# Optimization experiments

Hardware: AMD Instinct MI355X
Metric: run time of the kernel (lower is better)

Reference implementation:

```python
import jax, jax.numpy as jnp
import numpy as np

DIM = 1024; DEPTH = 2; DSTATE = 128; HEADDIM = 64; DCONV = 4; EXPAND = 2
DINNER = EXPAND * DIM; NHEADS = DINNER // HEADDIM
CONVCH = DINNER + 2 * DSTATE          # x, B, C channels fed through depthwise conv
DINPROJ = 2 * DINNER + 2 * DSTATE + NHEADS  # z, xBC, dt
VOCAB = 256; EPS = 1e-5
B, T = 2, 1024


def _causal_conv(x, w, b):
    # depthwise causal conv1d: x [B,T,C], w [C,K], b [C]
    K = w.shape[1]
    xp = jnp.pad(x, ((0, 0), (K - 1, 0), (0, 0)))
    y = jnp.broadcast_to(b, x.shape)
    for k in range(K):
        y = y + xp[:, k:k + x.shape[1], :] * w[:, k]
    return y


def _mamba2_layer(h, Wp, cw, cb, dtb, alog, Dd, gw, Wo):
    Bb, Tt, _ = h.shape
    zxbcdt = jnp.einsum('btd,pd->btp', h, Wp)   # [B,T,DINPROJ]
    z = zxbcdt[..., :DINNER]
    xBC = zxbcdt[..., DINNER:DINNER + CONVCH]
    dt_raw = zxbcdt[..., DINNER + CONVCH:]
    xBC = jax.nn.silu(_causal_conv(xBC, cw, cb))
    xs = xBC[..., :DINNER].reshape(Bb, Tt, NHEADS, HEADDIM)
    Bm = xBC[..., DINNER:DINNER + DSTATE]        # [B,T,N] (ngroups=1)
    Cm = xBC[..., DINNER + DSTATE:]              # [B,T,N]
    dt = jax.nn.softplus(dt_raw + dtb)           # [B,T,H]
    dA = jnp.exp(dt * (-jnp.exp(alog)))          # [B,T,H]

    def step(s, inps):
        da_t, dt_t, x_t, b_t, c_t = inps
        dbx = dt_t[:, :, None, None] * x_t[..., None] * b_t[:, None, None, :]
        s = da_t[:, :, None, None] * s + dbx     # [B,H,P,N]
        y = jnp.einsum('bhpn,bn->bhp', s, c_t)
        return s, y

    s0 = jnp.zeros((Bb, NHEADS, HEADDIM, DSTATE), h.dtype)
    seq = (jnp.moveaxis(dA, 1, 0), jnp.moveaxis(dt, 1, 0), jnp.moveaxis(xs, 1, 0),
           jnp.moveaxis(Bm, 1, 0), jnp.moveaxis(Cm, 1, 0))
    _, ys = jax.lax.scan(step, s0, seq)          # ys [T,B,H,P]
    y = jnp.moveaxis(ys, 0, 1) + Dd[:, None] * xs
    y = y.reshape(Bb, Tt, DINNER) * jax.nn.silu(z)   # gated RMSNorm (norm(y*silu(z)))
    y = y * jax.lax.rsqrt(jnp.mean(y * y, -1, keepdims=True) + EPS) * gw
    return jnp.einsum('bti,di->btd', y, Wo)


def setup_inputs() -> dict:
    key = jax.random.key(0)
    ks = jax.random.split(key, 8)
    s = 0.02
    inp = {}
    inp['x'] = jax.random.randint(ks[0], (B, T), 0, VOCAB)
    inp['embed'] = jax.random.normal(ks[1], (VOCAB, DIM)) * s
    inp['in_proj_w'] = jax.random.normal(ks[2], (DEPTH, DINPROJ, DIM)) * s
    inp['conv_w'] = jax.random.normal(ks[3], (DEPTH, CONVCH, DCONV)) * 0.2
    inp['conv_b'] = jnp.zeros((DEPTH, CONVCH))
    # dt_bias so softplus(dt) ~ [1e-3, 1e-1]
    inp['dt_bias'] = jax.random.uniform(ks[4], (DEPTH, NHEADS), minval=-4.6, maxval=-2.0)
    inp['A_log'] = jnp.log(jnp.broadcast_to(jnp.arange(1, NHEADS + 1, dtype=jnp.float32), (DEPTH, NHEADS)))
    inp['D'] = jnp.ones((DEPTH, NHEADS))
    inp['gnorm_w'] = jnp.ones((DEPTH, DINNER))
    inp['out_proj_w'] = jax.random.normal(ks[5], (DEPTH, DIM, DINNER)) * s
    inp['final_norm_w'] = jnp.ones((DIM,))
    return inp


def reference(x, embed, in_proj_w, conv_w, conv_b, dt_bias, A_log, D, gnorm_w, out_proj_w, final_norm_w):
    h = embed[x]                                  # [B,T,DIM]
    for l in range(DEPTH):
        h = h + _mamba2_layer(h, in_proj_w[l], conv_w[l], conv_b[l], dt_bias[l],
                              A_log[l], D[l], gnorm_w[l], out_proj_w[l])
    h = h * jax.lax.rsqrt(jnp.mean(h * h, -1, keepdims=True) + EPS) * final_norm_w
    return jnp.einsum('btd,vd->btv', h, embed)    # tied head -> logits [B,T,256]
```

## Files before the change

### kernel.cpp

```cpp
#include <hip/hip_runtime.h>
#include <hip/hip_bf16.h>

#define BT 2048
#define T_SEQ 1024
#define DIM 1024
#define DINNER 2048
#define DSTATE 128
#define HEADDIM 64
#define NHEADS 32
#define CONVCH 2304
#define DINPROJ 4384
#define EPS_F 1e-5f
#define NCHUNK 16

typedef __bf16 bf16x8 __attribute__((ext_vector_type(8)));
typedef float f32x4 __attribute__((ext_vector_type(4)));

__device__ __forceinline__ float b2f(unsigned short u) {
  union { unsigned int i; float f; } v; v.i = ((unsigned int)u) << 16; return v.f;
}
__device__ __forceinline__ unsigned short f2b(float f) {
  unsigned int x = __float_as_uint(f);
  return (unsigned short)((x + 0x7fffu + ((x >> 16) & 1u)) >> 16);
}

__device__ __forceinline__ void gload_lds16(const void* g, void* l) {
  __builtin_amdgcn_global_load_lds(
      (const __attribute__((address_space(1))) unsigned int*)g,
      (__attribute__((address_space(3))) unsigned int*)l, 16, 0, 0);
}

#define NWP_ELEM (2 * DINPROJ * DIM)
#define NWO_ELEM (2 * DIM * DINNER)
#define NEM_ELEM (256 * DIM)
#define NWP_BLK (NWP_ELEM / 4 / 256)
#define NWO_BLK (NWO_ELEM / 4 / 256)
#define NEM_BLK (NEM_ELEM / 4 / 256)
#define PRO_BLK (NWP_BLK + NWO_BLK + NEM_BLK + BT)

__global__ void prologue_k(const float* __restrict__ Wp, const float* __restrict__ Wo,
                           const float* __restrict__ emb, const float* __restrict__ gw,
                           unsigned short* __restrict__ Wp_b,
                           unsigned short* __restrict__ Wo_b,
                           unsigned short* __restrict__ emb_b,
                           const int* __restrict__ x,
                           float* __restrict__ h, unsigned short* __restrict__ hb) {
  int bid = blockIdx.x;
  if (bid < NWP_BLK) {
    int i = (bid * 256 + threadIdx.x) * 4;
    float4 v = *(const float4*)(Wp + i);
    Wp_b[i + 0] = f2b(v.x); Wp_b[i + 1] = f2b(v.y);
    Wp_b[i + 2] = f2b(v.z); Wp_b[i + 3] = f2b(v.w);
  } else if (bid < NWP_BLK + NWO_BLK) {
    int i = ((bid - NWP_BLK) * 256 + threadIdx.x) * 4;
    int li = i / (DIM * DINNER);
    int kk = i & (DINNER - 1);
    float4 v = *(const float4*)(Wo + i);
    float4 g = *(const float4*)(gw + li * DINNER + kk);
    Wo_b[i + 0] = f2b(v.x * g.x); Wo_b[i + 1] = f2b(v.y * g.y);
    Wo_b[i + 2] = f2b(v.z * g.z); Wo_b[i + 3] = f2b(v.w * g.w);
  } else if (bid < NWP_BLK + NWO_BLK + NEM_BLK) {
    int i = ((bid - NWP_BLK - NWO_BLK) * 256 + threadIdx.x) * 4;
    float4 v = *(const float4*)(emb + i);
    emb_b[i + 0] = f2b(v.x); emb_b[i + 1] = f2b(v.y);
    emb_b[i + 2] = f2b(v.z); emb_b[i + 3] = f2b(v.w);
  } else {
    int t = bid - (NWP_BLK + NWO_BLK + NEM_BLK);
    int tok = x[t];
    int d = threadIdx.x;
#pragma unroll
    for (int j = 0; j < 4; ++j, d += 256) {
      float v = emb[(size_t)tok * DIM + d];
      h[(size_t)t * DIM + d] = v;
      hb[(size_t)t * DIM + d] = f2b(v);
    }
  }
}

template <int MODE, int TM, int TN>
__global__ __launch_bounds__(256) void gemm_bt(
    const unsigned short* __restrict__ A,
    const unsigned short* __restrict__ Bw,
    int M, int N, int K,
    unsigned short* __restrict__ Cout,
    float* __restrict__ aux,
    unsigned short* __restrict__ aux2,
    const float* __restrict__ ssq) {
  constexpr int FM = TM / 32, FN = TN / 32;
  constexpr int JA = TM / 64, JB = TN / 64;
  constexpr int HA = TM * 32, HB = TN * 32;
  __shared__ __align__(16) unsigned short As[2 * HA];
  __shared__ __align__(16) unsigned short Bs[2 * HB];
  const int tid = threadIdx.x;
  const int lane = tid & 63;
  const int wave = tid >> 6;

  const int gx = gridDim.x, gy = gridDim.y;
  const int nwg = gx * gy;
  const int orig = (int)(blockIdx.y * gx + blockIdx.x);
  const int q = nwg >> 3, rr = nwg & 7;
  const int xcd = orig & 7, idx = orig >> 3;
  const int swz = (xcd < rr ? xcd * (q + 1) : rr * (q + 1) + (xcd - rr) * q) + idx;
  const int bxs = swz / gy;
  const int bys = swz - bxs * gy;
  const int m0 = bys * TM;
  const int n0 = bxs * TN;

  const int wm = (wave >> 1) * (TM / 2);
  const int wn = (wave & 1) * (TN / 2);
  const int quad = lane >> 4;
  const int r = lane & 15;

  f32x4 acc[FM][FN];
#pragma unroll
  for (int i = 0; i < FM; ++i)
#pragma unroll
    for (int j = 0; j < FN; ++j) acc[i][j] = f32x4{0.f, 0.f, 0.f, 0.f};

  const int rowt = tid >> 2, colt = (tid & 3) * 8;
  const unsigned short* aG[JA];
  unsigned short* aD[JA];
  const unsigned short* bG[JB];
  unsigned short* bD[JB];
#pragma unroll
  for (int j = 0; j < JA; ++j) {
    aG[j] = A + (size_t)(m0 + rowt + j * 64) * K + colt;
    aD[j] = As + wave * 512 + j * 2048;
  }
#pragma unroll
  for (int j = 0; j < JB; ++j) {
    int rb = n0 + rowt + j * 64; if (rb >= N) rb = N - 1;
    bG[j] = Bw + (size_t)rb * K + colt;
    bD[j] = Bs + wave * 512 + j * 2048;
  }

#pragma unroll
  for (int j = 0; j < JA; ++j) gload_lds16(aG[j], aD[j]);
#pragma unroll
  for (int j = 0; j < JB; ++j) gload_lds16(bG[j], bD[j]);
  __syncthreads();

  int cur = 0;
  for (int k0 = 0; k0 < K; k0 += 32) {
    const int nxt = cur ^ 1;
    if (k0 + 32 < K) {
#pragma unroll
      for (int j = 0; j < JA; ++j) gload_lds16(aG[j] + k0 + 32, aD[j] + nxt * HA);
#pragma unroll
      for (int j = 0; j < JB; ++j) gload_lds16(bG[j] + k0 + 32, bD[j] + nxt * HB);
    }
    const bf16x8* ap = (const bf16x8*)(As + cur * HA);
    const bf16x8* bp = (const bf16x8*)(Bs + cur * HB);
    bf16x8 af[FM], bfr[FN];
#pragma unroll
    for (int mt = 0; mt < FM; ++mt) af[mt] = ap[(wm + mt * 16 + r) * 4 + quad];
#pragma unroll
    for (int nt = 0; nt < FN; ++nt) bfr[nt] = bp[(wn + nt * 16 + r) * 4 + quad];
#pragma unroll
    for (int mt = 0; mt < FM; ++mt)
#pragma unroll
      for (int nt = 0; nt < FN; ++nt)
        acc[mt][nt] = __builtin_amdgcn_mfma_f32_16x16x32_bf16(af[mt], bfr[nt], acc[mt][nt], 0, 0, 0);
    __syncthreads();
    cur = nxt;
  }

#pragma unroll
  for (int mt = 0; mt < FM; ++mt) {
#pragma unroll
    for (int nt = 0; nt < FN; ++nt) {
#pragma unroll
      for (int i = 0; i < 4; ++i) {
        int gm = m0 + wm + mt * 16 + quad * 4 + i;
        int gn = n0 + wn + nt * 16 + r;
        if (gn < N) {
          float v = acc[mt][nt][i];
          if (MODE == 0) {
            Cout[(size_t)gm * N + gn] = f2b(v);
            if (gn >= DINNER + CONVCH)
              aux[(size_t)gm * NHEADS + (gn - (DINNER + CONVCH))] = v;
          } else if (MODE == 1) {
            float scl = rsqrtf(ssq[gm] * (1.f / DINNER) + EPS_F);
            size_t o = (size_t)gm * N + gn;
            float hnv = aux[o] + v * scl;
            aux[o] = hnv;
            aux2[o] = f2b(hnv);
          } else {
            aux[(size_t)gm * N + gn] = v;
          }
        }
      }
    }
  }
}

__global__ void conv_k(const unsigned short* __restrict__ zx,
                       const float* __restrict__ cw,
                       const float* __restrict__ cb,
                       unsigned short* __restrict__ xbc,
                       unsigned short* __restrict__ bcb,
                       const float* __restrict__ dtraw,
                       const float* __restrict__ dtb,
                       const float* __restrict__ alog,
                       float* __restrict__ dtf,
                       float* __restrict__ lnAf,
                       float* __restrict__ ssq) {
  int t = blockIdx.x;
  int tt = t & (T_SEQ - 1);
  if (threadIdx.x == 0) ssq[t] = 0.f;
  if (threadIdx.x < NHEADS) {
    int h = threadIdx.x;
    float xx = dtraw[t * NHEADS + h] + dtb[h];
    float sp = (xx > 20.f) ? xx : log1pf(expf(xx));
    dtf[t * NHEADS + h] = sp;
    lnAf[t * NHEADS + h] = -sp * expf(alog[h]);
  }
  for (int c = threadIdx.x; c < CONVCH; c += 256) {
    float acc = cb[c];
#pragma unroll
    for (int k = 0; k < 4; ++k) {
      int tp = tt - 3 + k;
      if (tp >= 0)
        acc += b2f(zx[(size_t)(t - 3 + k) * DINPROJ + DINNER + c]) * cw[c * 4 + k];
    }
    float s = acc / (1.f + expf(-acc));
    unsigned short sb = f2b(s);
    xbc[(size_t)t * CONVCH + c] = sb;
    if (c >= DINNER) bcb[(size_t)t * 256 + (c - DINNER)] = sb;
  }
}

__global__ __launch_bounds__(256) void ssd_intra(
    const unsigned short* __restrict__ bcb,
    const unsigned short* __restrict__ xbc,
    const float* __restrict__ dtf, const float* __restrict__ lnAf,
    unsigned short* __restrict__ y1buf, unsigned short* __restrict__ SL,
    float* __restrict__ dtot) {
  const int bi = blockIdx.x;
  const int c = bi & 15;
  const int h = (bi >> 4) & 31;
  const int b = bi >> 9;
  const int tid = threadIdx.x;
  const int w = tid >> 6, l = tid & 63, r = l & 15, quad = l >> 4;
  const size_t tok0 = (size_t)b * T_SEQ + c * 64;

  __shared__ __align__(16) unsigned short BCs[64 * 264];
  __shared__ __align__(16) unsigned short Xrow[64 * 72];
  __shared__ __align__(16) unsigned short XTs[64 * 72];
  __shared__ __align__(16) unsigned short BWT[128 * 72];
  __shared__ __align__(16) unsigned short Ms[64 * 72];
  __shared__ float cumL[64], dtL[64], wsL[64];

#pragma unroll
  for (int i = 0; i < 8; ++i) {
    int idx = tid + i * 256;
    int row = idx >> 5, col = (idx & 31) * 8;
    uint4 v = *(const uint4*)(bcb + (tok0 + row) * 256 + col);
    *(uint4*)(BCs + row * 264 + col) = v;
  }
#pragma unroll
  for (int i = 0; i < 2; ++i) {
    int idx = tid + i * 256;
    int u = idx >> 3, pc = (idx & 7) * 8;
    uint4 v = *(const uint4*)(xbc + (tok0 + u) * CONVCH + h * HEADDIM + pc);
    *(uint4*)(Xrow + u * 72 + pc) = v;
  }
  if (tid < 64) {
    float dt = dtf[(tok0 + tid) * NHEADS + h];
    float v = lnAf[(tok0 + tid) * NHEADS + h];
    dtL[tid] = dt;
#pragma unroll
    for (int off = 1; off < 64; off <<= 1) {
      float u = __shfl_up(v, off, 64);
      if (tid >= off) v += u;
    }
    cumL[tid] = v;
    float tot = __shfl(v, 63, 64);
    wsL[tid] = dt * expf(tot - v);
    if (tid == 63) dtot[bi] = expf(tot);
  }
  __syncthreads();

#pragma unroll
  for (int i = 0; i < 2; ++i) {
    int idx = tid + i * 256;
    int p = idx >> 3, ug = (idx & 7) * 8;
    unsigned short tA[8];
#pragma unroll
    for (int j = 0; j < 8; ++j) tA[j] = Xrow[(ug + j) * 72 + p];
    *(uint4*)(XTs + p * 72 + ug) = *(uint4*)tA;
  }

  {
    const int n = tid >> 1;
    const int ug = (tid & 1) * 32;
    unsigned short eb[32];
#pragma unroll
    for (int j = 0; j < 32; ++j)
      eb[j] = f2b(b2f(BCs[(ug + j) * 264 + n]) * wsL[ug + j]);
#pragma unroll
    for (int qq = 0; qq < 4; ++qq)
      *(uint4*)(BWT + n * 72 + ug + qq * 8) = *(uint4*)(eb + qq * 8);
  }

  f32x4 g[4];
#pragma unroll
  for (int nt = 0; nt < 4; ++nt) g[nt] = f32x4{0.f, 0.f, 0.f, 0.f};
#pragma unroll
  for (int kk = 0; kk < 4; ++kk) {
    bf16x8 afr = *(const bf16x8*)(BCs + (w * 16 + r) * 264 + 128 + kk * 32 + quad * 8);
#pragma unroll
    for (int nt = 0; nt < 4; ++nt) {
      bf16x8 bfr = *(const bf16x8*)(BCs + (nt * 16 + r) * 264 + kk * 32 + quad * 8);
      g[nt] = __builtin_amdgcn_mfma_f32_16x16x32_bf16(afr, bfr, g[nt], 0, 0, 0);
    }
  }
#pragma unroll
  for (int nt = 0; nt < 4; ++nt) {
#pragma unroll
    for (int i = 0; i < 4; ++i) {
      int t_ = w * 16 + quad * 4 + i;
      int u_ = nt * 16 + r;
      float wv = (u_ <= t_) ? expf(cumL[t_] - cumL[u_]) * dtL[u_] : 0.f;
      Ms[t_ * 72 + u_] = f2b(g[nt][i] * wv);
    }
  }
  __syncthreads();

  f32x4 y1[4];
#pragma unroll
  for (int nt = 0; nt < 4; ++nt) y1[nt] = f32x4{0.f, 0.f, 0.f, 0.f};
#pragma unroll
  for (int kk = 0; kk < 2; ++kk) {
    bf16x8 afr = *(const bf16x8*)(Ms + (w * 16 + r) * 72 + kk * 32 + quad * 8);
#pragma unroll
    for (int nt = 0; nt < 4; ++nt) {
      bf16x8 bfr = *(const bf16x8*)(XTs + (nt * 16 + r) * 72 + kk * 32 + quad * 8);
      y1[nt] = __builtin_amdgcn_mfma_f32_16x16x32_bf16(afr, bfr, y1[nt], 0, 0, 0);
    }
  }
#pragma unroll
  for (int nt = 0; nt < 4; ++nt)
#pragma unroll
    for (int i = 0; i < 4; ++i) {
      int t_ = w * 16 + quad * 4 + i, p_ = nt * 16 + r;
      y1buf[((size_t)bi * 64 + t_) * 64 + p_] = f2b(y1[nt][i]);
    }

  f32x4 sl[8];
#pragma unroll
  for (int nt = 0; nt < 8; ++nt) sl[nt] = f32x4{0.f, 0.f, 0.f, 0.f};
#pragma unroll
  for (int kk = 0; kk < 2; ++kk) {
    bf16x8 afr = *(const bf16x8*)(XTs + (w * 16 + r) * 72 + kk * 32 + quad * 8);
#pragma unroll
    for (int nt = 0; nt < 8; ++nt) {
      bf16x8 bfr = *(const bf16x8*)(BWT + (nt * 16 + r) * 72 + kk * 32 + quad * 8);
      sl[nt] = __builtin_amdgcn_mfma_f32_16x16x32_bf16(afr, bfr, sl[nt], 0, 0, 0);
    }
  }
#pragma unroll
  for (int nt = 0; nt < 8; ++nt)
#pragma unroll
    for (int i = 0; i < 4; ++i) {
      int p_ = w * 16 + quad * 4 + i, n_ = nt * 16 + r;
      SL[((size_t)bi * 64 + p_) * 128 + n_] = f2b(sl[nt][i]);
    }
}

__global__ void ssd_state(unsigned short* __restrict__ SL,
                          const float* __restrict__ dtot) {
  int gidx = blockIdx.x * 256 + threadIdx.x;
  int n4 = (gidx & 31) * 4;
  int p = (gidx >> 5) & 63;
  int bh = gidx >> 11;
  float sx = 0.f, sy = 0.f, sz = 0.f, sw = 0.f;
  for (int c = 0; c < NCHUNK; ++c) {
    size_t off = ((size_t)(bh * 16 + c) * 64 + p) * 128 + n4;
    uint2 lv = *(uint2*)(SL + off);
    float d = dtot[bh * 16 + c];
    uint2 sv;
    sv.x = (unsigned)f2b(sx) | ((unsigned)f2b(sy) << 16);
    sv.y = (unsigned)f2b(sz) | ((unsigned)f2b(sw) << 16);
    *(uint2*)(SL + off) = sv;
    sx = d * sx + b2f(lv.x & 0xffff);
    sy = d * sy + b2f(lv.x >> 16);
    sz = d * sz + b2f(lv.y & 0xffff);
    sw = d * sw + b2f(lv.y >> 16);
  }
}

__global__ __launch_bounds__(256) void ssd_inter(
    const unsigned short* __restrict__ bcb,
    const unsigned short* __restrict__ SL,
    const unsigned short* __restrict__ y1buf,
    const unsigned short* __restrict__ xbc,
    const unsigned short* __restrict__ zx,
    const float* __restrict__ lnAf,
    const float* __restrict__ Dw,
    unsigned short* __restrict__ yg,
    float* __restrict__ ssq) {
  const int bi = blockIdx.x;
  const int c = bi & 15, h = (bi >> 4) & 31, b = bi >> 9;
  const int tid = threadIdx.x;
  const int w = tid >> 6, l = tid & 63, r = l & 15, quad = l >> 4;
  const size_t tok0 = (size_t)b * T_SEQ + c * 64;

  __shared__ __align__(16) unsigned short Cs[64 * 136];
  __shared__ __align__(16) unsigned short Sp[64 * 136];
  __shared__ __align__(16) float Yf[64 * 68];
  __shared__ float cumL[64];

#pragma unroll
  for (int i = 0; i < 4; ++i) {
    int idx = tid + i * 256;
    int row = idx >> 4, col = (idx & 15) * 8;
    uint4 v = *(const uint4*)(bcb + (tok0 + row) * 256 + 128 + col);
    *(uint4*)(Cs + row * 136 + col) = v;
    uint4 s = *(const uint4*)(SL + ((size_t)bi * 64 + row) * 128 + col);
    *(uint4*)(Sp + row * 136 + col) = s;
  }
  if (tid < 64) {
    float v = lnAf[(tok0 + tid) * NHEADS + h];
#pragma unroll
    for (int off = 1; off < 64; off <<= 1) {
      float u = __shfl_up(v, off, 64);
      if (tid >= off) v += u;
    }
    cumL[tid] = v;
  }
  __syncthreads();

  f32x4 yi[4];
#pragma unroll
  for (int nt = 0; nt < 4; ++nt) yi[nt] = f32x4{0.f, 0.f, 0.f, 0.f};
#pragma unroll
  for (int kk = 0; kk < 4; ++kk) {
    bf16x8 afr = *(const bf16x8*)(Cs + (w * 16 + r) * 136 + kk * 32 + quad * 8);
#pragma unroll
    for (int nt = 0; nt < 4; ++nt) {
      bf16x8 bfr = *(const bf16x8*)(Sp + (nt * 16 + r) * 136 + kk * 32 + quad * 8);
      yi[nt] = __builtin_amdgcn_mfma_f32_16x16x32_bf16(afr, bfr, yi[nt], 0, 0, 0);
    }
  }
#pragma unroll
  for (int nt = 0; nt < 4; ++nt)
#pragma unroll
    for (int i = 0; i < 4; ++i) {
      int t_ = w * 16 + quad * 4 + i, p_ = nt * 16 + r;
      float y1 = b2f(y1buf[((size_t)bi * 64 + t_) * 64 + p_]);
      Yf[t_ * 68 + p_] = y1 + expf(cumL[t_]) * yi[nt][i];
    }
  __syncthreads();

  const float Dh = Dw[h];
  const int t_ = tid >> 2, pg = (tid & 3) * 16;
  const size_t tok = tok0 + t_;
  union { uint4 q[2]; unsigned short u[16]; } xv, zv, ov;
  xv.q[0] = *(const uint4*)(xbc + tok * CONVCH + h * 64 + pg);
  xv.q[1] = *(const uint4*)(xbc + tok * CONVCH + h * 64 + pg + 8);
  zv.q[0] = *(const uint4*)(zx + tok * DINPROJ + h * 64 + pg);
  zv.q[1] = *(const uint4*)(zx + tok * DINPROJ + h * 64 + pg + 8);
  float ssf = 0.f;
#pragma unroll
  for (int j = 0; j < 16; ++j) {
    float y = Yf[t_ * 68 + pg + j] + Dh * b2f(xv.u[j]);
    float zf = b2f(zv.u[j]);
    float yg_f = y * (zf / (1.f + expf(-zf)));
    ov.u[j] = f2b(yg_f);
    ssf += yg_f * yg_f;
  }
  *(uint4*)(yg + tok * DINNER + h * 64 + pg) = ov.q[0];
  *(uint4*)(yg + tok * DINNER + h * 64 + pg + 8) = ov.q[1];
  ssf += __shfl_xor(ssf, 1, 64);
  ssf += __shfl_xor(ssf, 2, 64);
  if ((tid & 3) == 0) atomicAdd(&ssq[tok], ssf);
}

__global__ void rmsfinal_k(const float* __restrict__ hf,
                           const float* __restrict__ w,
                           unsigned short* __restrict__ out) {
  int t = blockIdx.x;
  int base = threadIdx.x * 4;
  float4 v = *(const float4*)(hf + (size_t)t * DIM + base);
  float ss = v.x * v.x + v.y * v.y + v.z * v.z + v.w * v.w;
#pragma unroll
  for (int o = 32; o > 0; o >>= 1) ss += __shfl_xor(ss, o, 64);
  __shared__ float red[4];
  if ((threadIdx.x & 63) == 0) red[threadIdx.x >> 6] = ss;
  __syncthreads();
  ss = red[0] + red[1] + red[2] + red[3];
  float scale = rsqrtf(ss * (1.f / DIM) + EPS_F);
  out[(size_t)t * DIM + base + 0] = f2b(v.x * scale * w[base + 0]);
  out[(size_t)t * DIM + base + 1] = f2b(v.y * scale * w[base + 1]);
  out[(size_t)t * DIM + base + 2] = f2b(v.z * scale * w[base + 2]);
  out[(size_t)t * DIM + base + 3] = f2b(v.w * scale * w[base + 3]);
}

extern "C" void kernel_launch(void* const* d_in, const int* in_sizes, int n_in,
                              void* d_out, int out_size, void* d_ws, size_t ws_size,
                              hipStream_t stream) {
  const int*   x    = (const int*)d_in[0];
  const float* emb  = (const float*)d_in[1];
  const float* Wp   = (const float*)d_in[2];
  const float* cw   = (const float*)d_in[3];
  const float* cb   = (const float*)d_in[4];
  const float* dtb  = (const float*)d_in[5];
  const float* alog = (const float*)d_in[6];
  const float* Dw   = (const float*)d_in[7];
  const float* gw   = (const float*)d_in[8];
  const float* Wo   = (const float*)d_in[9];
  const float* fnw  = (const float*)d_in[10];

  char* w = (char*)d_ws;
  auto alloc = [&](size_t bytes) {
    char* p = w; w += (bytes + 255) & ~(size_t)255; return p;
  };
  float* h_f32          = (float*)alloc((size_t)BT * DIM * 4);
  unsigned short* hb    = (unsigned short*)alloc((size_t)BT * DIM * 2);
  unsigned short* zx    = (unsigned short*)alloc((size_t)BT * DINPROJ * 2);
  float* dtraw          = (float*)alloc((size_t)BT * NHEADS * 4);
  float* dtf            = (float*)alloc((size_t)BT * NHEADS * 4);
  float* lnAf           = (float*)alloc((size_t)BT * NHEADS * 4);
  unsigned short* xbc   = (unsigned short*)alloc((size_t)BT * CONVCH * 2);
  unsigned short* bcb   = (unsigned short*)alloc((size_t)BT * 256 * 2);
  unsigned short* SL    = (unsigned short*)alloc((size_t)1024 * 64 * 128 * 2);
  unsigned short* y1buf = (unsigned short*)alloc((size_t)1024 * 64 * 64 * 2);
  float* dtot           = (float*)alloc((size_t)1024 * 4);
  unsigned short* yg    = (unsigned short*)alloc((size_t)BT * DINNER * 2);
  float* ssq            = (float*)alloc((size_t)BT * 4);
  unsigned short* hn    = (unsigned short*)alloc((size_t)BT * DIM * 2);
  unsigned short* Wp_b  = (unsigned short*)alloc((size_t)2 * DINPROJ * DIM * 2);
  unsigned short* Wo_b  = (unsigned short*)alloc((size_t)2 * DIM * DINNER * 2);
  unsigned short* emb_b = (unsigned short*)alloc((size_t)256 * DIM * 2 + 256);

  prologue_k<<<PRO_BLK, 256, 0, stream>>>(Wp, Wo, emb, gw, Wp_b, Wo_b, emb_b, x, h_f32, hb);

  for (int l = 0; l < 2; ++l) {
    const unsigned short* Wpl = Wp_b + (size_t)l * DINPROJ * DIM;
    const unsigned short* Wol = Wo_b + (size_t)l * DIM * DINNER;
    const float* cwl   = cw + (size_t)l * CONVCH * 4;
    const float* cbl   = cb + (size_t)l * CONVCH;
    const float* dtbl  = dtb + l * NHEADS;
    const float* alogl = alog + l * NHEADS;
    const float* Dwl   = Dw + l * NHEADS;

    gemm_bt<0, 128, 128><<<dim3(35, 16), 256, 0, stream>>>(hb, Wpl, BT, DINPROJ, DIM, zx, dtraw, nullptr, nullptr);
    conv_k<<<BT, 256, 0, stream>>>(zx, cwl, cbl, xbc, bcb, dtraw, dtbl, alogl, dtf, lnAf, ssq);
    ssd_intra<<<1024, 256, 0, stream>>>(bcb, xbc, dtf, lnAf, y1buf, SL, dtot);
    ssd_state<<<512, 256, 0, stream>>>(SL, dtot);
    ssd_inter<<<1024, 256, 0, stream>>>(bcb, SL, y1buf, xbc, zx, lnAf, Dwl, yg, ssq);
    gemm_bt<1, 64, 64><<<dim3(16, 32), 256, 0, stream>>>(yg, Wol, BT, DIM, DINNER, nullptr, h_f32, hb, ssq);
  }

  rmsfinal_k<<<BT, 256, 0, stream>>>(h_f32, fnw, hn);
  gemm_bt<2, 64, 64><<<dim3(4, 32), 256, 0, stream>>>(hn, emb_b, BT, 256, DIM,
                                                      nullptr, (float*)d_out, nullptr, nullptr);
}
```

Baseline: 364.6 us.

## Fuse final RMSNorm into out-proj epilogue and logits GEMM

Removes the separate final RMSNorm kernel. The residual-update epilogue of the out-projection GEMM now accumulates per-row sums of squares of the new hidden state via shuffles and atomics. The final norm weight is folded into the bf16 embedding at prologue time, and the logits GEMM scales each row by the rsqrt of that sum. This saves one launch and a read and write of the hidden state, at the cost of extra atomics in the GEMM epilogue and normalizing after the bf16 matmul instead of before.

Measured after the change: 368.7 us. No clear change (+1.1%).

```diff
diff --git a/kernel.cpp b/kernel.cpp
--- a/kernel.cpp
+++ b/kernel.cpp
@@ -40,6 +40,7 @@
 
 __global__ void prologue_k(const float* __restrict__ Wp, const float* __restrict__ Wo,
                            const float* __restrict__ emb, const float* __restrict__ gw,
+                           const float* __restrict__ fnw,
                            unsigned short* __restrict__ Wp_b,
                            unsigned short* __restrict__ Wo_b,
                            unsigned short* __restrict__ emb_b,
@@ -61,9 +62,11 @@
     Wo_b[i + 2] = f2b(v.z * g.z); Wo_b[i + 3] = f2b(v.w * g.w);
   } else if (bid < NWP_BLK + NWO_BLK + NEM_BLK) {
     int i = ((bid - NWP_BLK - NWO_BLK) * 256 + threadIdx.x) * 4;
+    int kk = i & (DIM - 1);
     float4 v = *(const float4*)(emb + i);
-    emb_b[i + 0] = f2b(v.x); emb_b[i + 1] = f2b(v.y);
-    emb_b[i + 2] = f2b(v.z); emb_b[i + 3] = f2b(v.w);
+    float4 g = *(const float4*)(fnw + kk);
+    emb_b[i + 0] = f2b(v.x * g.x); emb_b[i + 1] = f2b(v.y * g.y);
+    emb_b[i + 2] = f2b(v.z * g.z); emb_b[i + 3] = f2b(v.w * g.w);
   } else {
     int t = bid - (NWP_BLK + NWO_BLK + NEM_BLK);
     int tok = x[t];
@@ -85,7 +88,8 @@
     unsigned short* __restrict__ Cout,
     float* __restrict__ aux,
     unsigned short* __restrict__ aux2,
-    const float* __restrict__ ssq) {
+    const float* __restrict__ ssq,
+    float* __restrict__ ssqo) {
   constexpr int FM = TM / 32, FN = TN / 32;
   constexpr int JA = TM / 64, JB = TN / 64;
   constexpr int HA = TM * 32, HB = TN * 32;
@@ -163,6 +167,14 @@
         acc[mt][nt] = __builtin_amdgcn_mfma_f32_16x16x32_bf16(af[mt], bfr[nt], acc[mt][nt], 0, 0, 0);
     __syncthreads();
     cur = nxt;
+  }
+
+  float rs[FM][4];
+  if (MODE == 1) {
+#pragma unroll
+    for (int mt = 0; mt < FM; ++mt)
+#pragma unroll
+      for (int i = 0; i < 4; ++i) rs[mt][i] = 0.f;
   }
 
 #pragma unroll
@@ -185,12 +197,31 @@
             float hnv = aux[o] + v * scl;
             aux[o] = hnv;
             aux2[o] = f2b(hnv);
+            rs[mt][i] += hnv * hnv;
           } else {
-            aux[(size_t)gm * N + gn] = v;
+            float scl = rsqrtf(ssq[gm] * (1.f / DIM) + EPS_F);
+            aux[(size_t)gm * N + gn] = v * scl;
           }
         }
       }
     }
+  }
+
+  if (MODE == 1) {
+#pragma unroll
+    for (int mt = 0; mt < FM; ++mt)
+#pragma unroll
+      for (int i = 0; i < 4; ++i) {
+        float s = rs[mt][i];
+        s += __shfl_xor(s, 1, 64);
+        s += __shfl_xor(s, 2, 64);
+        s += __shfl_xor(s, 4, 64);
+        s += __shfl_xor(s, 8, 64);
+        if (r == 0) {
+          int gm = m0 + wm + mt * 16 + quad * 4 + i;
+          atomicAdd(&ssqo[gm], s);
+        }
+      }
   }
 }
 
@@ -204,10 +235,12 @@
                        const float* __restrict__ alog,
                        float* __restrict__ dtf,
                        float* __restrict__ lnAf,
-                       float* __restrict__ ssq) {
+                       float* __restrict__ ssq,
+                       float* __restrict__ ssqh) {
   int t = blockIdx.x;
   int tt = t & (T_SEQ - 1);
   if (threadIdx.x == 0) ssq[t] = 0.f;
+  if (threadIdx.x == 1) ssqh[t] = 0.f;
   if (threadIdx.x < NHEADS) {
     int h = threadIdx.x;
     float xx = dtraw[t * NHEADS + h] + dtb[h];
@@ -477,26 +510,6 @@
   if ((tid & 3) == 0) atomicAdd(&ssq[tok], ssf);
 }
 
-__global__ void rmsfinal_k(const float* __restrict__ hf,
-                           const float* __restrict__ w,
-                           unsigned short* __restrict__ out) {
-  int t = blockIdx.x;
-  int base = threadIdx.x * 4;
-  float4 v = *(const float4*)(hf + (size_t)t * DIM + base);
-  float ss = v.x * v.x + v.y * v.y + v.z * v.z + v.w * v.w;
-#pragma unroll
-  for (int o = 32; o > 0; o >>= 1) ss += __shfl_xor(ss, o, 64);
-  __shared__ float red[4];
-  if ((threadIdx.x & 63) == 0) red[threadIdx.x >> 6] = ss;
-  __syncthreads();
-  ss = red[0] + red[1] + red[2] + red[3];
-  float scale = rsqrtf(ss * (1.f / DIM) + EPS_F);
-  out[(size_t)t * DIM + base + 0] = f2b(v.x * scale * w[base + 0]);
-  out[(size_t)t * DIM + base + 1] = f2b(v.y * scale * w[base + 1]);
-  out[(size_t)t * DIM + base + 2] = f2b(v.z * scale * w[base + 2]);
-  out[(size_t)t * DIM + base + 3] = f2b(v.w * scale * w[base + 3]);
-}
-
 extern "C" void kernel_launch(void* const* d_in, const int* in_sizes, int n_in,
                               void* d_out, int out_size, void* d_ws, size_t ws_size,
                               hipStream_t stream) {
@@ -529,12 +542,12 @@
   float* dtot           = (float*)alloc((size_t)1024 * 4);
   unsigned short* yg    = (unsigned short*)alloc((size_t)BT * DINNER * 2);
   float* ssq            = (float*)alloc((size_t)BT * 4);
-  unsigned short* hn    = (unsigned short*)alloc((size_t)BT * DIM * 2);
+  float* ssqh           = (float*)alloc((size_t)BT * 4);
   unsigned short* Wp_b  = (unsigned short*)alloc((size_t)2 * DINPROJ * DIM * 2);
   unsigned short* Wo_b  = (unsigned short*)alloc((size_t)2 * DIM * DINNER * 2);
   unsigned short* emb_b = (unsigned short*)alloc((size_t)256 * DIM * 2 + 256);
 
-  prologue_k<<<PRO_BLK, 256, 0, stream>>>(Wp, Wo, emb, gw, Wp_b, Wo_b, emb_b, x, h_f32, hb);
+  prologue_k<<<PRO_BLK, 256, 0, stream>>>(Wp, Wo, emb, gw, fnw, Wp_b, Wo_b, emb_b, x, h_f32, hb);
 
   for (int l = 0; l < 2; ++l) {
     const unsigned short* Wpl = Wp_b + (size_t)l * DINPROJ * DIM;
@@ -545,15 +558,14 @@
     const float* alogl = alog + l * NHEADS;
     const float* Dwl   = Dw + l * NHEADS;
 
-    gemm_bt<0, 128, 128><<<dim3(35, 16), 256, 0, stream>>>(hb, Wpl, BT, DINPROJ, DIM, zx, dtraw, nullptr, nullptr);
-    conv_k<<<BT, 256, 0, stream>>>(zx, cwl, cbl, xbc, bcb, dtraw, dtbl, alogl, dtf, lnAf, ssq);
+    gemm_bt<0, 128, 128><<<dim3(35, 16), 256, 0, stream>>>(hb, Wpl, BT, DINPROJ, DIM, zx, dtraw, nullptr, nullptr, nullptr);
+    conv_k<<<BT, 256, 0, stream>>>(zx, cwl, cbl, xbc, bcb, dtraw, dtbl, alogl, dtf, lnAf, ssq, ssqh);
     ssd_intra<<<1024, 256, 0, stream>>>(bcb, xbc, dtf, lnAf, y1buf, SL, dtot);
     ssd_state<<<512, 256, 0, stream>>>(SL, dtot);
     ssd_inter<<<1024, 256, 0, stream>>>(bcb, SL, y1buf, xbc, zx, lnAf, Dwl, yg, ssq);
-    gemm_bt<1, 64, 64><<<dim3(16, 32), 256, 0, stream>>>(yg, Wol, BT, DIM, DINNER, nullptr, h_f32, hb, ssq);
-  }
-
-  rmsfinal_k<<<BT, 256, 0, stream>>>(h_f32, fnw, hn);
-  gemm_bt<2, 64, 64><<<dim3(4, 32), 256, 0, stream>>>(hn, emb_b, BT, 256, DIM,
-                                                      nullptr, (float*)d_out, nullptr, nullptr);
-}
+    gemm_bt<1, 64, 64><<<dim3(16, 32), 256, 0, stream>>>(yg, Wol, BT, DIM, DINNER, nullptr, h_f32, hb, ssq, ssqh);
+  }
+
+  gemm_bt<2, 64, 64><<<dim3(4, 32), 256, 0, stream>>>(hb, emb_b, BT, 256, DIM,
+                                                      nullptr, (float*)d_out, nullptr, ssqh, nullptr);
+}
```
